# Kernel tuning notes

Measured on AMD Instinct MI355X. Metric: run time of the kernel, lower is better.

## Reference

```python
import jax, jax.numpy as jnp
import numpy as np

N_EMBD = 512
BLOCK_SIZE = 512
NUM_HEADS = 8
HEAD_SIZE = 64
ROPE_BASE = 10000.0


def apply_rope(x):
    # x: [B, H, T, D]; rotates interleaved pairs with position = token index.
    B, H, T, D = x.shape
    half = D // 2
    inv_freq = 1.0 / (ROPE_BASE ** (jnp.arange(half, dtype=jnp.float32) * 2.0 / D))
    ang = jnp.arange(T, dtype=jnp.float32)[:, None] * inv_freq[None, :]  # [T, half]
    cos = jnp.cos(ang).astype(x.dtype)  # [T, half]
    sin = jnp.sin(ang).astype(x.dtype)
    x1 = x[..., 0::2]  # [B,H,T,half]
    x2 = x[..., 1::2]
    o1 = x1 * cos - x2 * sin
    o2 = x2 * cos + x1 * sin
    return jnp.stack([o1, o2], axis=-1).reshape(B, H, T, D)


def setup_inputs() -> dict:
    key = jax.random.key(0)
    ks = jax.random.split(key, 6)
    B, T, C = 32, 512, N_EMBD
    HD = NUM_HEADS * HEAD_SIZE
    s_in = 1.0 / np.sqrt(C)
    s_out = 1.0 / np.sqrt(HD)
    return {
        "x": jax.random.normal(ks[0], (B, T, C), dtype=jnp.float32),
        "Wq": jax.random.normal(ks[1], (C, HD), dtype=jnp.float32) * s_in,
        "Wk": jax.random.normal(ks[2], (C, HD), dtype=jnp.float32) * s_in,
        "Wv": jax.random.normal(ks[3], (C, HD), dtype=jnp.float32) * s_in,
        "Wo": jax.random.normal(ks[4], (HD, C), dtype=jnp.float32) * s_out,
        "bo": jax.random.normal(ks[5], (C,), dtype=jnp.float32) * 0.01,
    }


def reference(x, Wq, Wk, Wv, Wo, bo):
    B, T, C = x.shape
    H, D = NUM_HEADS, HEAD_SIZE
    # projections -> [B, H, T, D]
    q = (x @ Wq).reshape(B, T, H, D).transpose(0, 2, 1, 3)
    k = (x @ Wk).reshape(B, T, H, D).transpose(0, 2, 1, 3)
    v = (x @ Wv).reshape(B, T, H, D).transpose(0, 2, 1, 3)
    q = apply_rope(q)
    k = apply_rope(k)
    scale = 1.0 / np.sqrt(D)
    wei = jnp.einsum('bhqd,bhkd->bhqk', q, k) * scale  # [B,H,T,T]
    causal = jnp.tril(jnp.ones((T, T), dtype=bool))
    wei = jnp.where(causal, wei, -jnp.inf)
    wei = jax.nn.softmax(wei, axis=-1)
    # dropout omitted (eval mode / deterministic baseline)
    out = jnp.einsum('bhqk,bhkd->bhqd', wei, v)  # [B,H,T,D]
    out = out.transpose(0, 2, 1, 3).reshape(B, T, H * D)
    return out @ Wo + bo
```

## Files before the change

kernel.cpp:

```cpp
#include <hip/hip_runtime.h>

#define TSEQ 512
#define CDIM 512
#define NH 8
#define HS 64
#define BBATCH 32
#define MROWS (BBATCH * TSEQ)

typedef unsigned short u16;
typedef __bf16 bf16x8 __attribute__((ext_vector_type(8)));
typedef float f32x4 __attribute__((ext_vector_type(4)));
typedef float f32x16 __attribute__((ext_vector_type(16)));

__device__ __forceinline__ u16 f2b(float f) {
  union { float f; unsigned u; } v; v.f = f;
  unsigned r = (v.u + 0x7fffu + ((v.u >> 16) & 1u)) >> 16;
  return (u16)r;
}

__device__ __forceinline__ void gload_lds16(const u16* g, u16* l) {
  __builtin_amdgcn_global_load_lds(
      (const __attribute__((address_space(1))) void*)g,
      (__attribute__((address_space(3))) void*)l, 16, 0, 0);
}


__global__ __launch_bounds__(256) void conv_x(const float* __restrict__ x,
                                              u16* __restrict__ A2) {
  __shared__ __align__(16) u16 tile[128][136];
  const int tid = threadIdx.x;
  const int m0 = blockIdx.x * 128;
  const int cc = blockIdx.y;
#pragma unroll
  for (int i = 0; i < 16; ++i) {
    int idx = i * 256 + tid;
    int ml = idx >> 5, c4 = idx & 31;
    float4 v = *reinterpret_cast<const float4*>(
        x + (size_t)(m0 + ml) * CDIM + cc * 128 + c4 * 4);
    ushort4 o; o.x = f2b(v.x); o.y = f2b(v.y); o.z = f2b(v.z); o.w = f2b(v.w);
    *reinterpret_cast<ushort4*>(&tile[ml][c4 * 4]) = o;
  }
  __syncthreads();
#pragma unroll
  for (int i = 0; i < 8; ++i) {
    int uid = i * 256 + tid;
    int kb = uid >> 7, ml = uid & 127;
    int4 v = *reinterpret_cast<const int4*>(&tile[ml][kb * 8]);
    *reinterpret_cast<int4*>(A2 + ((size_t)(cc * 16 + kb) * MROWS + m0 + ml) * 8) = v;
  }
}

__global__ __launch_bounds__(256) void transpose_w(const float* __restrict__ wq,
                                                   const float* __restrict__ wk,
                                                   const float* __restrict__ wv,
                                                   const float* __restrict__ wo,
                                                   u16* __restrict__ B2,
                                                   u16* __restrict__ B2o) {
  __shared__ __align__(16) u16 tile[64][136];
  const int tid = threadIdx.x;
  int mat = blockIdx.z;
  const float* src = (mat == 0) ? wq : (mat == 1) ? wk : (mat == 2) ? wv : wo;
  u16* dst = (mat < 3) ? (B2 + (size_t)mat * 64 * 512 * 8) : B2o;
  const int k0 = blockIdx.x * 64, n0 = blockIdx.y * 128;
#pragma unroll
  for (int i = 0; i < 8; ++i) {
    int idx = i * 256 + tid;
    int kl = idx >> 5, c4 = idx & 31;
    float4 v = *reinterpret_cast<const float4*>(
        src + (size_t)(k0 + kl) * CDIM + n0 + c4 * 4);
    ushort4 o; o.x = f2b(v.x); o.y = f2b(v.y); o.z = f2b(v.z); o.w = f2b(v.w);
    *reinterpret_cast<ushort4*>(&tile[kl][c4 * 4]) = o;
  }
  __syncthreads();
#pragma unroll
  for (int i = 0; i < 4; ++i) {
    int uid = i * 256 + tid;
    int kb = uid >> 7, nl = uid & 127;
    ushort4 lo, hi;
    lo.x = tile[kb * 8 + 0][nl]; lo.y = tile[kb * 8 + 1][nl];
    lo.z = tile[kb * 8 + 2][nl]; lo.w = tile[kb * 8 + 3][nl];
    hi.x = tile[kb * 8 + 4][nl]; hi.y = tile[kb * 8 + 5][nl];
    hi.z = tile[kb * 8 + 6][nl]; hi.w = tile[kb * 8 + 7][nl];
    u16* d = dst + ((size_t)(k0 / 8 + kb) * 512 + n0 + nl) * 8;
    *reinterpret_cast<ushort4*>(d) = lo;
    *reinterpret_cast<ushort4*>(d + 4) = hi;
  }
}

__global__ __launch_bounds__(256) void rope_tab(float* __restrict__ cosT,
                                                float* __restrict__ sinT) {
  int i = blockIdx.x * 256 + threadIdx.x;
  int t = i >> 5, f = i & 31;
  float inv = __powf(10000.0f, -(float)f / 32.0f);
  float ang = (float)t * inv;
  cosT[i] = cosf(ang);
  sinT[i] = sinf(ang);
}

__global__ __launch_bounds__(256) void vt_t(const u16* __restrict__ Vb,
                                            u16* __restrict__ VT) {
  __shared__ __align__(16) u16 tile[64][72];
  const int bh = blockIdx.x;
  const int b = bh >> 3, h = bh & 7;
  const int tt = blockIdx.y;
  const int tid = threadIdx.x;
#pragma unroll
  for (int p = 0; p < 2; ++p) {
    int tl = (tid >> 3) + p * 32;
    int dc = tid & 7;
    const u16* src = Vb + (size_t)(b * TSEQ + tt * 64 + tl) * CDIM + h * HS + dc * 8;
    ushort4 v0 = *reinterpret_cast<const ushort4*>(src);
    ushort4 v1 = *reinterpret_cast<const ushort4*>(src + 4);
    tile[dc * 8 + 0][tl] = v0.x; tile[dc * 8 + 1][tl] = v0.y;
    tile[dc * 8 + 2][tl] = v0.z; tile[dc * 8 + 3][tl] = v0.w;
    tile[dc * 8 + 4][tl] = v1.x; tile[dc * 8 + 5][tl] = v1.y;
    tile[dc * 8 + 6][tl] = v1.z; tile[dc * 8 + 7][tl] = v1.w;
  }
  __syncthreads();
#pragma unroll
  for (int p = 0; p < 2; ++p) {
    int d = (tid >> 3) + p * 32;
    int tc = tid & 7;
    int4 vdat = *reinterpret_cast<const int4*>(&tile[d][tc * 8]);
    *reinterpret_cast<int4*>(VT + (size_t)(bh * HS + d) * TSEQ + tt * 64 + tc * 8) = vdat;
  }
}

__global__ __launch_bounds__(256, 2) void qkv_gemm(const u16* __restrict__ A2,
                                                   const u16* __restrict__ B2,
                                                   const float* __restrict__ cosT,
                                                   const float* __restrict__ sinT,
                                                   u16* __restrict__ Qb,
                                                   u16* __restrict__ Kb,
                                                   u16* __restrict__ Vb) {
  __shared__ __align__(16) u16 lds[3][8192];
  const int tid = threadIdx.x;
  const int lane = tid & 63;
  const int l31 = lane & 31, hh = lane >> 5;
  const int wid = tid >> 6;
  const int wmb = (wid >> 1) * 64, wnb = (wid & 1) * 64;
  const int m0 = blockIdx.x * 128;
  const int n0 = blockIdx.y * 128;
  const int mat = n0 >> 9;
  const int nc0 = n0 & 511;
  const u16* B2m = B2 + (size_t)mat * (64 * 512 * 8);

  f32x16 acc[2][2] = {};

  auto stage = [&](int buf, int t) {
#pragma unroll
    for (int c = 0; c < 2; ++c) {
      int u = c * 256 + tid;
      int kb = u >> 7, ml = u & 127;
      gload_lds16(A2 + ((size_t)(t * 4 + kb) * MROWS + m0 + ml) * 8,
                  &lds[buf][u * 8]);
    }
#pragma unroll
    for (int c = 0; c < 2; ++c) {
      int u = c * 256 + tid;
      int kb = u >> 7, nl = u & 127;
      gload_lds16(B2m + ((size_t)(t * 4 + kb) * 512 + nc0 + nl) * 8,
                  &lds[buf][4096 + u * 8]);
    }
  };

  stage(0, 0);
  stage(1, 1);
#pragma unroll
  for (int t = 0; t < 16; ++t) {
    const int cur = t % 3;
    if (t + 2 < 16) {
      stage((t + 2) % 3, t + 2);
      asm volatile("s_waitcnt vmcnt(8)" ::: "memory");
    } else if (t + 2 == 16) {
      asm volatile("s_waitcnt vmcnt(4)" ::: "memory");
    } else {
      asm volatile("s_waitcnt vmcnt(0)" ::: "memory");
    }
    __builtin_amdgcn_sched_barrier(0);
    __builtin_amdgcn_s_barrier();
    __builtin_amdgcn_sched_barrier(0);
    const u16* LA = &lds[cur][0];
    const u16* LB = &lds[cur][4096];
#pragma unroll
    for (int ks = 0; ks < 2; ++ks) {
      int kb2 = ks * 2 + hh;
      bf16x8 a0 = *reinterpret_cast<const bf16x8*>(LA + (kb2 * 128 + wmb + l31) * 8);
      bf16x8 a1 = *reinterpret_cast<const bf16x8*>(LA + (kb2 * 128 + wmb + 32 + l31) * 8);
      bf16x8 b0 = *reinterpret_cast<const bf16x8*>(LB + (kb2 * 128 + wnb + l31) * 8);
      bf16x8 b1 = *reinterpret_cast<const bf16x8*>(LB + (kb2 * 128 + wnb + 32 + l31) * 8);
      acc[0][0] = __builtin_amdgcn_mfma_f32_32x32x16_bf16(a0, b0, acc[0][0], 0, 0, 0);
      acc[0][1] = __builtin_amdgcn_mfma_f32_32x32x16_bf16(a0, b1, acc[0][1], 0, 0, 0);
      acc[1][0] = __builtin_amdgcn_mfma_f32_32x32x16_bf16(a1, b0, acc[1][0], 0, 0, 0);
      acc[1][1] = __builtin_amdgcn_mfma_f32_32x32x16_bf16(a1, b1, acc[1][1], 0, 0, 0);
    }
    __builtin_amdgcn_sched_barrier(0);
    __builtin_amdgcn_s_barrier();
    __builtin_amdgcn_sched_barrier(0);
  }

  if (mat < 2) {
    u16* dst = (mat == 0) ? Qb : Kb;
    const float qs = (mat == 0) ? 0.125f * 1.4426950408889634f : 1.0f;
#pragma unroll
    for (int nr = 0; nr < 2; ++nr) {
      int nc = nc0 + wnb + nr * 32 + l31;
      int fi = (nc & 63) >> 1;
      int odd = nc & 1;
#pragma unroll
      for (int mr = 0; mr < 2; ++mr)
#pragma unroll
        for (int r = 0; r < 16; ++r) {
          int row = m0 + wmb + mr * 32 + (r & 3) + 8 * (r >> 2) + 4 * hh;
          int tq = row & (TSEQ - 1);
          float v = acc[mr][nr][r];
          float o = __shfl_xor(v, 1);
          float c = cosT[tq * 32 + fi], sn = sinT[tq * 32 + fi];
          float res = odd ? (v * c + o * sn) : (v * c - o * sn);
          dst[(size_t)row * CDIM + nc] = f2b(res * qs);
        }
    }
  } else {
#pragma unroll
    for (int nr = 0; nr < 2; ++nr) {
      int nc = nc0 + wnb + nr * 32 + l31;
#pragma unroll
      for (int mr = 0; mr < 2; ++mr)
#pragma unroll
        for (int r = 0; r < 16; ++r) {
          int row = m0 + wmb + mr * 32 + (r & 3) + 8 * (r >> 2) + 4 * hh;
          Vb[(size_t)row * CDIM + nc] = f2b(acc[mr][nr][r]);
        }
    }
  }
}

__global__ __launch_bounds__(128, 4) void attn_kern(const u16* __restrict__ Qb,
                                                    const u16* __restrict__ Kb,
                                                    const u16* __restrict__ VT,
                                                    u16* __restrict__ A2out) {
  const int lane = threadIdx.x & 63, wid = threadIdx.x >> 6;
  const int l31 = lane & 31, hh = lane >> 5;
  const int bh = blockIdx.x, b = bh >> 3, h = bh & 7;
  const int q0 = blockIdx.y * 64 + wid * 32;

  bf16x8 qf[4];
  const u16* qbase = Qb + (size_t)(b * TSEQ + q0 + l31) * CDIM + h * HS + hh * 8;
#pragma unroll
  for (int ds = 0; ds < 4; ++ds)
    qf[ds] = *reinterpret_cast<const bf16x8*>(qbase + ds * 16);

  float lsum = 0.0f;
  f32x16 of[2] = {};

  const int nkt = (q0 >> 5) + 1;
  for (int kt = 0; kt < nkt; ++kt) {
    f32x16 s = {};
    const u16* kr = Kb + (size_t)(b * TSEQ + kt * 32 + l31) * CDIM + h * HS + hh * 8;
    __builtin_amdgcn_s_setprio(1);
#pragma unroll
    for (int ds = 0; ds < 4; ++ds) {
      bf16x8 kf = *reinterpret_cast<const bf16x8*>(kr + ds * 16);
      s = __builtin_amdgcn_mfma_f32_32x32x16_bf16(kf, qf[ds], s, 0, 0, 0);
    }
    __builtin_amdgcn_s_setprio(0);
    float p[16];
    if (kt == nkt - 1) {
#pragma unroll
      for (int r = 0; r < 16; ++r) {
        int kk = (r & 3) + 8 * (r >> 2) + 4 * hh;
        p[r] = (kk > l31) ? 0.0f : exp2f(s[r]);
      }
    } else {
#pragma unroll
      for (int r = 0; r < 16; ++r) p[r] = exp2f(s[r]);
    }
    float ts = 0.0f;
#pragma unroll
    for (int r = 0; r < 16; ++r) ts += p[r];
    ts += __shfl_xor(ts, 32);
    lsum += ts;

    unsigned w0, w1, w2, w3, w4, w5, w6, w7;
    asm("v_cvt_pk_bf16_f32 %0, %1, %2" : "=v"(w0) : "v"(p[0]),  "v"(p[1]));
    asm("v_cvt_pk_bf16_f32 %0, %1, %2" : "=v"(w1) : "v"(p[2]),  "v"(p[3]));
    asm("v_cvt_pk_bf16_f32 %0, %1, %2" : "=v"(w2) : "v"(p[4]),  "v"(p[5]));
    asm("v_cvt_pk_bf16_f32 %0, %1, %2" : "=v"(w3) : "v"(p[6]),  "v"(p[7]));
    asm("v_cvt_pk_bf16_f32 %0, %1, %2" : "=v"(w4) : "v"(p[8]),  "v"(p[9]));
    asm("v_cvt_pk_bf16_f32 %0, %1, %2" : "=v"(w5) : "v"(p[10]), "v"(p[11]));
    asm("v_cvt_pk_bf16_f32 %0, %1, %2" : "=v"(w6) : "v"(p[12]), "v"(p[13]));
    asm("v_cvt_pk_bf16_f32 %0, %1, %2" : "=v"(w7) : "v"(p[14]), "v"(p[15]));
    asm("v_permlane32_swap_b32 %0, %1" : "+v"(w0), "+v"(w2));
    asm("v_permlane32_swap_b32 %0, %1" : "+v"(w1), "+v"(w3));
    asm("v_permlane32_swap_b32 %0, %1" : "+v"(w4), "+v"(w6));
    asm("v_permlane32_swap_b32 %0, %1" : "+v"(w5), "+v"(w7));
    union { unsigned u[4]; bf16x8 v; } pb0, pb1;
    pb0.u[0] = w0; pb0.u[1] = w1; pb0.u[2] = w2; pb0.u[3] = w3;
    pb1.u[0] = w4; pb1.u[1] = w5; pb1.u[2] = w6; pb1.u[3] = w7;

    const u16* vr = VT + (size_t)(bh * HS + l31) * TSEQ + kt * 32 + hh * 8;
    bf16x8 vf00 = *reinterpret_cast<const bf16x8*>(vr);
    bf16x8 vf01 = *reinterpret_cast<const bf16x8*>(vr + 16);
    bf16x8 vf10 = *reinterpret_cast<const bf16x8*>(vr + 32 * TSEQ);
    bf16x8 vf11 = *reinterpret_cast<const bf16x8*>(vr + 32 * TSEQ + 16);
    __builtin_amdgcn_s_setprio(1);
    of[0] = __builtin_amdgcn_mfma_f32_32x32x16_bf16(vf00, pb0.v, of[0], 0, 0, 0);
    of[0] = __builtin_amdgcn_mfma_f32_32x32x16_bf16(vf01, pb1.v, of[0], 0, 0, 0);
    of[1] = __builtin_amdgcn_mfma_f32_32x32x16_bf16(vf10, pb0.v, of[1], 0, 0, 0);
    of[1] = __builtin_amdgcn_mfma_f32_32x32x16_bf16(vf11, pb1.v, of[1], 0, 0, 0);
    __builtin_amdgcn_s_setprio(0);
  }

  float inv = 1.0f / lsum;
  const int grow = b * TSEQ + q0 + l31;
#pragma unroll
  for (int dt = 0; dt < 2; ++dt)
#pragma unroll
    for (int i = 0; i < 8; ++i) {
      ushort2 st;
      st.x = f2b(of[dt][2 * i] * inv);
      st.y = f2b(of[dt][2 * i + 1] * inv);
      int kb = h * 8 + dt * 4 + ((2 * i) >> 2);
      int off = ((2 * i) & 3) + 4 * hh;
      *reinterpret_cast<ushort2*>(
          A2out + ((size_t)kb * MROWS + grow) * 8 + off) = st;
    }
}

__global__ __launch_bounds__(256, 2) void out_gemm(const u16* __restrict__ A2,
                                                   const u16* __restrict__ B2o,
                                                   const float* __restrict__ bias,
                                                   float* __restrict__ out) {
  __shared__ __align__(16) u16 lds[3][8192];
  const int tid = threadIdx.x;
  const int lane = tid & 63;
  const int l31 = lane & 31, hh = lane >> 5;
  const int wid = tid >> 6;
  const int wmb = (wid >> 1) * 64, wnb = (wid & 1) * 64;
  const int m0 = blockIdx.x * 128;
  const int n0 = blockIdx.y * 128;

  f32x16 acc[2][2] = {};

  auto stage = [&](int buf, int t) {
#pragma unroll
    for (int c = 0; c < 2; ++c) {
      int u = c * 256 + tid;
      int kb = u >> 7, ml = u & 127;
      gload_lds16(A2 + ((size_t)(t * 4 + kb) * MROWS + m0 + ml) * 8,
                  &lds[buf][u * 8]);
    }
#pragma unroll
    for (int c = 0; c < 2; ++c) {
      int u = c * 256 + tid;
      int kb = u >> 7, nl = u & 127;
      gload_lds16(B2o + ((size_t)(t * 4 + kb) * 512 + n0 + nl) * 8,
                  &lds[buf][4096 + u * 8]);
    }
  };

  stage(0, 0);
  stage(1, 1);
#pragma unroll
  for (int t = 0; t < 16; ++t) {
    const int cur = t % 3;
    if (t + 2 < 16) {
      stage((t + 2) % 3, t + 2);
      asm volatile("s_waitcnt vmcnt(8)" ::: "memory");
    } else if (t + 2 == 16) {
      asm volatile("s_waitcnt vmcnt(4)" ::: "memory");
    } else {
      asm volatile("s_waitcnt vmcnt(0)" ::: "memory");
    }
    __builtin_amdgcn_sched_barrier(0);
    __builtin_amdgcn_s_barrier();
    __builtin_amdgcn_sched_barrier(0);
    const u16* LA = &lds[cur][0];
    const u16* LB = &lds[cur][4096];
#pragma unroll
    for (int ks = 0; ks < 2; ++ks) {
      int kb2 = ks * 2 + hh;
      bf16x8 a0 = *reinterpret_cast<const bf16x8*>(LA + (kb2 * 128 + wmb + l31) * 8);
      bf16x8 a1 = *reinterpret_cast<const bf16x8*>(LA + (kb2 * 128 + wmb + 32 + l31) * 8);
      bf16x8 b0 = *reinterpret_cast<const bf16x8*>(LB + (kb2 * 128 + wnb + l31) * 8);
      bf16x8 b1 = *reinterpret_cast<const bf16x8*>(LB + (kb2 * 128 + wnb + 32 + l31) * 8);
      acc[0][0] = __builtin_amdgcn_mfma_f32_32x32x16_bf16(a0, b0, acc[0][0], 0, 0, 0);
      acc[0][1] = __builtin_amdgcn_mfma_f32_32x32x16_bf16(a0, b1, acc[0][1], 0, 0, 0);
      acc[1][0] = __builtin_amdgcn_mfma_f32_32x32x16_bf16(a1, b0, acc[1][0], 0, 0, 0);
      acc[1][1] = __builtin_amdgcn_mfma_f32_32x32x16_bf16(a1, b1, acc[1][1], 0, 0, 0);
    }
    __builtin_amdgcn_sched_barrier(0);
    __builtin_amdgcn_s_barrier();
    __builtin_amdgcn_sched_barrier(0);
  }

#pragma unroll
  for (int nr = 0; nr < 2; ++nr) {
    int col = n0 + wnb + nr * 32 + l31;
    float bv = bias[col];
#pragma unroll
    for (int mr = 0; mr < 2; ++mr)
#pragma unroll
      for (int r = 0; r < 16; ++r) {
        int row = m0 + wmb + mr * 32 + (r & 3) + 8 * (r >> 2) + 4 * hh;
        out[(size_t)row * CDIM + col] = acc[mr][nr][r] + bv;
      }
  }
}

extern "C" void kernel_launch(void* const* d_in, const int* in_sizes, int n_in,
                              void* d_out, int out_size, void* d_ws, size_t ws_size,
                              hipStream_t stream) {
  const float* x  = (const float*)d_in[0];
  const float* Wq = (const float*)d_in[1];
  const float* Wk = (const float*)d_in[2];
  const float* Wv = (const float*)d_in[3];
  const float* Wo = (const float*)d_in[4];
  const float* bo = (const float*)d_in[5];
  float* out = (float*)d_out;

  char* p = (char*)d_ws;
  const size_t big = (size_t)MROWS * CDIM * 2;
  u16* A2x  = (u16*)p; p += big;
  u16* B2   = (u16*)p; p += (size_t)3 * 64 * 512 * 8 * 2;
  u16* B2o  = (u16*)p; p += (size_t)64 * 512 * 8 * 2;
  float* cosT = (float*)p; p += (size_t)TSEQ * 32 * 4;
  float* sinT = (float*)p; p += (size_t)TSEQ * 32 * 4;
  u16* Qb   = (u16*)p; p += big;
  u16* Kb   = (u16*)p; p += big;
  u16* VT   = (u16*)p; p += big;
  u16* Vb   = (u16*)p; p += big;

  hipLaunchKernelGGL(conv_x, dim3(MROWS / 128, 4), dim3(256), 0, stream, x, A2x);
  hipLaunchKernelGGL(transpose_w, dim3(8, 4, 4), dim3(256), 0, stream,
                     Wq, Wk, Wv, Wo, B2, B2o);
  hipLaunchKernelGGL(rope_tab, dim3(TSEQ * 32 / 256), dim3(256), 0, stream, cosT, sinT);
  hipLaunchKernelGGL(qkv_gemm, dim3(MROWS / 128, 1536 / 128), dim3(256), 0, stream,
                     A2x, B2, cosT, sinT, Qb, Kb, Vb);
  hipLaunchKernelGGL(vt_t, dim3(BBATCH * NH, TSEQ / 64), dim3(256), 0, stream, Vb, VT);
  hipLaunchKernelGGL(attn_kern, dim3(BBATCH * NH, TSEQ / 64), dim3(128), 0, stream,
                     Qb, Kb, VT, A2x);
  hipLaunchKernelGGL(out_gemm, dim3(MROWS / 128, CDIM / 128), dim3(256), 0, stream,
                     A2x, B2o, bo, out);
}
```

Before: 109.1 us.

## Store K and V in MFMA-fragment-major layout for contiguous attention loads

The QKV GEMM epilogue now writes roped K directly in a per-(batch, head, 32-key tile) fragment layout, so each lane's four K fragments sit in 64 contiguous bytes. The V transpose kernel writes V in the same fragment-major layout. The attention kernel then reads K and V with one contiguous per-lane stream per tile instead of strided row reads. The aim is better coalescing and fewer cache lines touched in the attention inner loop. In exchange, the K epilogue scatters its stores more, which may cost write efficiency in the GEMM.

```diff
diff --git a/kernel.cpp b/kernel.cpp
--- a/kernel.cpp
+++ b/kernel.cpp
@@ -98,7 +98,7 @@
 }
 
 __global__ __launch_bounds__(256) void vt_t(const u16* __restrict__ Vb,
-                                            u16* __restrict__ VT) {
+                                            u16* __restrict__ Vf) {
   __shared__ __align__(16) u16 tile[64][72];
   const int bh = blockIdx.x;
   const int b = bh >> 3, h = bh & 7;
@@ -117,12 +117,15 @@
     tile[dc * 8 + 6][tl] = v1.z; tile[dc * 8 + 7][tl] = v1.w;
   }
   __syncthreads();
+  const int lane = tid & 63, u = tid >> 6;
+  const int l31f = lane & 31, hhf = lane >> 5;
 #pragma unroll
   for (int p = 0; p < 2; ++p) {
-    int d = (tid >> 3) + p * 32;
-    int tc = tid & 7;
-    int4 vdat = *reinterpret_cast<const int4*>(&tile[d][tc * 8]);
-    *reinterpret_cast<int4*>(VT + (size_t)(bh * HS + d) * TSEQ + tt * 64 + tc * 8) = vdat;
+    int d = l31f + (u >> 1) * 32;
+    int toff = p * 32 + hhf * 8 + (u & 1) * 16;
+    int4 v = *reinterpret_cast<const int4*>(&tile[d][toff]);
+    *reinterpret_cast<int4*>(
+        Vf + (((size_t)bh * 16 + tt * 2 + p) * 64 + lane) * 32 + u * 8) = v;
   }
 }
 
@@ -131,7 +134,7 @@
                                                    const float* __restrict__ cosT,
                                                    const float* __restrict__ sinT,
                                                    u16* __restrict__ Qb,
-                                                   u16* __restrict__ Kb,
+                                                   u16* __restrict__ Kf,
                                                    u16* __restrict__ Vb) {
   __shared__ __align__(16) u16 lds[3][8192];
   const int tid = threadIdx.x;
@@ -199,9 +202,8 @@
     __builtin_amdgcn_sched_barrier(0);
   }
 
-  if (mat < 2) {
-    u16* dst = (mat == 0) ? Qb : Kb;
-    const float qs = (mat == 0) ? 0.125f * 1.4426950408889634f : 1.0f;
+  if (mat == 0) {
+    const float qs = 0.125f * 1.4426950408889634f;
 #pragma unroll
     for (int nr = 0; nr < 2; ++nr) {
       int nc = nc0 + wnb + nr * 32 + l31;
@@ -217,7 +219,32 @@
           float o = __shfl_xor(v, 1);
           float c = cosT[tq * 32 + fi], sn = sinT[tq * 32 + fi];
           float res = odd ? (v * c + o * sn) : (v * c - o * sn);
-          dst[(size_t)row * CDIM + nc] = f2b(res * qs);
+          Qb[(size_t)row * CDIM + nc] = f2b(res * qs);
+        }
+    }
+  } else if (mat == 1) {
+    const int bidx = m0 >> 9;
+#pragma unroll
+    for (int nr = 0; nr < 2; ++nr) {
+      int nc = nc0 + wnb + nr * 32 + l31;
+      int h2 = nc >> 6, e = nc & 63;
+      int fi = e >> 1;
+      int odd = nc & 1;
+      int laneHi = ((e >> 3) & 1) * 32;
+      int idx = ((e >> 4) * 8) + (e & 7);
+#pragma unroll
+      for (int mr = 0; mr < 2; ++mr)
+#pragma unroll
+        for (int r = 0; r < 16; ++r) {
+          int row = m0 + wmb + mr * 32 + (r & 3) + 8 * (r >> 2) + 4 * hh;
+          int tq = row & (TSEQ - 1);
+          float v = acc[mr][nr][r];
+          float o = __shfl_xor(v, 1);
+          float c = cosT[tq * 32 + fi], sn = sinT[tq * 32 + fi];
+          float res = odd ? (v * c + o * sn) : (v * c - o * sn);
+          size_t addr = ((((size_t)(bidx * 8 + h2) * 16 + (tq >> 5)) * 64)
+                         + laneHi + (tq & 31)) * 32 + idx;
+          Kf[addr] = f2b(res);
         }
     }
   } else {
@@ -236,8 +263,8 @@
 }
 
 __global__ __launch_bounds__(128, 4) void attn_kern(const u16* __restrict__ Qb,
-                                                    const u16* __restrict__ Kb,
-                                                    const u16* __restrict__ VT,
+                                                    const u16* __restrict__ Kf,
+                                                    const u16* __restrict__ Vf,
                                                     u16* __restrict__ A2out) {
   const int lane = threadIdx.x & 63, wid = threadIdx.x >> 6;
   const int l31 = lane & 31, hh = lane >> 5;
@@ -255,12 +282,12 @@
 
   const int nkt = (q0 >> 5) + 1;
   for (int kt = 0; kt < nkt; ++kt) {
+    const u16* kfr = Kf + (((size_t)bh * 16 + kt) * 64 + lane) * 32;
     f32x16 s = {};
-    const u16* kr = Kb + (size_t)(b * TSEQ + kt * 32 + l31) * CDIM + h * HS + hh * 8;
     __builtin_amdgcn_s_setprio(1);
 #pragma unroll
     for (int ds = 0; ds < 4; ++ds) {
-      bf16x8 kf = *reinterpret_cast<const bf16x8*>(kr + ds * 16);
+      bf16x8 kf = *reinterpret_cast<const bf16x8*>(kfr + ds * 8);
       s = __builtin_amdgcn_mfma_f32_32x32x16_bf16(kf, qf[ds], s, 0, 0, 0);
     }
     __builtin_amdgcn_s_setprio(0);
@@ -298,11 +325,11 @@
     pb0.u[0] = w0; pb0.u[1] = w1; pb0.u[2] = w2; pb0.u[3] = w3;
     pb1.u[0] = w4; pb1.u[1] = w5; pb1.u[2] = w6; pb1.u[3] = w7;
 
-    const u16* vr = VT + (size_t)(bh * HS + l31) * TSEQ + kt * 32 + hh * 8;
-    bf16x8 vf00 = *reinterpret_cast<const bf16x8*>(vr);
-    bf16x8 vf01 = *reinterpret_cast<const bf16x8*>(vr + 16);
-    bf16x8 vf10 = *reinterpret_cast<const bf16x8*>(vr + 32 * TSEQ);
-    bf16x8 vf11 = *reinterpret_cast<const bf16x8*>(vr + 32 * TSEQ + 16);
+    const u16* vfr = Vf + (((size_t)bh * 16 + kt) * 64 + lane) * 32;
+    bf16x8 vf00 = *reinterpret_cast<const bf16x8*>(vfr);
+    bf16x8 vf01 = *reinterpret_cast<const bf16x8*>(vfr + 8);
+    bf16x8 vf10 = *reinterpret_cast<const bf16x8*>(vfr + 16);
+    bf16x8 vf11 = *reinterpret_cast<const bf16x8*>(vfr + 24);
     __builtin_amdgcn_s_setprio(1);
     of[0] = __builtin_amdgcn_mfma_f32_32x32x16_bf16(vf00, pb0.v, of[0], 0, 0, 0);
     of[0] = __builtin_amdgcn_mfma_f32_32x32x16_bf16(vf01, pb1.v, of[0], 0, 0, 0);
@@ -427,8 +454,8 @@
   float* cosT = (float*)p; p += (size_t)TSEQ * 32 * 4;
   float* sinT = (float*)p; p += (size_t)TSEQ * 32 * 4;
   u16* Qb   = (u16*)p; p += big;
-  u16* Kb   = (u16*)p; p += big;
-  u16* VT   = (u16*)p; p += big;
+  u16* Kf   = (u16*)p; p += big;
+  u16* Vf   = (u16*)p; p += big;
   u16* Vb   = (u16*)p; p += big;
 
   hipLaunchKernelGGL(conv_x, dim3(MROWS / 128, 4), dim3(256), 0, stream, x, A2x);
@@ -436,10 +463,10 @@
                      Wq, Wk, Wv, Wo, B2, B2o);
   hipLaunchKernelGGL(rope_tab, dim3(TSEQ * 32 / 256), dim3(256), 0, stream, cosT, sinT);
   hipLaunchKernelGGL(qkv_gemm, dim3(MROWS / 128, 1536 / 128), dim3(256), 0, stream,
-                     A2x, B2, cosT, sinT, Qb, Kb, Vb);
-  hipLaunchKernelGGL(vt_t, dim3(BBATCH * NH, TSEQ / 64), dim3(256), 0, stream, Vb, VT);
+                     A2x, B2, cosT, sinT, Qb, Kf, Vb);
+  hipLaunchKernelGGL(vt_t, dim3(BBATCH * NH, TSEQ / 64), dim3(256), 0, stream, Vb, Vf);
   hipLaunchKernelGGL(attn_kern, dim3(BBATCH * NH, TSEQ / 64), dim3(128), 0, stream,
-                     Qb, Kb, VT, A2x);
+                     Qb, Kf, Vf, A2x);
   hipLaunchKernelGGL(out_gemm, dim3(MROWS / 128, CDIM / 128), dim3(256), 0, stream,
                      A2x, B2o, bo, out);
 }
```

After: 98.72 us. 9.5% less time.
